# Optimization experiments

Measured on AMD Instinct MI355X. Metric: run time of the kernel, lower is better.

Reference implementation:

```python
import jax, jax.numpy as jnp
import numpy as np
import math

B, S, H = 2, 2048, 1024
NH, HD = 16, 64  # num heads, head dim; NH*HD == H


def setup_inputs() -> dict:
    key = jax.random.key(0)
    k1, k2, k3 = jax.random.split(key, 3)
    hidden_states = jax.random.normal(k1, (B, S, H), dtype=jnp.float32)
    # causal multiplicative mask [1,1,S,S], 1.0 where attending is allowed
    mask = jnp.tril(jnp.ones((S, S), dtype=jnp.float32))[None, None]
    W_qkv = jax.random.normal(k2, (H, 3 * H), dtype=jnp.float32) * (1.0 / math.sqrt(H))
    b_qkv = jnp.zeros((3 * H,), dtype=jnp.float32)
    W_out = jax.random.normal(k3, (H, H), dtype=jnp.float32) * (1.0 / math.sqrt(H))
    b_out = jnp.zeros((H,), dtype=jnp.float32)
    return {"hidden_states": hidden_states, "mask": mask, "W_qkv": W_qkv,
            "b_qkv": b_qkv, "W_out": W_out, "b_out": b_out}


def reference(hidden_states, mask, W_qkv, b_qkv, W_out, b_out):
    b, s, h = hidden_states.shape
    # fused QKV projection then split into contiguous thirds (split_tensor_along_last_dim)
    qkv = jnp.einsum('bsh,hd->bsd', hidden_states, W_qkv) + b_qkv
    q, k, v = jnp.split(qkv, 3, axis=-1)
    # [b, s, nh*hd] -> [b, nh, s, hd]
    def to_heads(t):
        return t.reshape(b, s, NH, HD).transpose(0, 2, 1, 3)
    q, k, v = to_heads(q), to_heads(k), to_heads(v)
    q = q / jnp.sqrt(jnp.float32(HD))  # scaling_attention_score=True
    scores = jnp.einsum('bhqd,bhkd->bhqk', q, k)  # [b,nh,s,s]
    # multiplicative mask + large-negative bias trick from standard_attention
    scores = scores * mask - 10000.0 * (1.0 - mask)
    probs = jax.nn.softmax(scores, axis=-1)
    ctx = jnp.einsum('bhqk,bhkd->bhqd', probs, v)
    ctx = ctx.transpose(0, 2, 1, 3).reshape(b, s, h)  # [b, s, nh*hd]
    return jnp.einsum('bsh,hd->bsd', ctx, W_out) + b_out
```

## Files before the change

### kernel.cpp

```cpp
#include <hip/hip_runtime.h>
#include <cstdint>
#include <cstddef>

#define NHEAD 16
#define HDIM 64
#define SEQ 2048
#define BATCH 2
#define HID 1024

typedef __bf16 bf16x8 __attribute__((ext_vector_type(8)));
typedef __bf16 bf16x2_t __attribute__((ext_vector_type(2)));
typedef float f32x4 __attribute__((ext_vector_type(4)));

__device__ __forceinline__ unsigned short f2bf(float f) {
    union { float f; unsigned u; } v; v.f = f;
    unsigned r = v.u + 0x7fffu + ((v.u >> 16) & 1u);
    return (unsigned short)(r >> 16);
}

__device__ __forceinline__ unsigned pk_bf16(float a, float b) {
#if __has_builtin(__builtin_amdgcn_cvt_pk_bf16_f32)
    bf16x2_t p = __builtin_amdgcn_cvt_pk_bf16_f32(a, b);
    return __builtin_bit_cast(unsigned, p);
#else
    return (unsigned)f2bf(a) | ((unsigned)f2bf(b) << 16);
#endif
}

__global__ __launch_bounds__(256) void convert_f32_bf16(
    const float* __restrict__ in, unsigned short* __restrict__ out, int n) {
    int i = (blockIdx.x * 256 + threadIdx.x) * 8;
    if (i >= n) return;
    float4 a = *(const float4*)(in + i);
    float4 b = *(const float4*)(in + i + 4);
    uint4 o;
    o.x = pk_bf16(a.x, a.y);
    o.y = pk_bf16(a.z, a.w);
    o.z = pk_bf16(b.x, b.y);
    o.w = pk_bf16(b.z, b.w);
    *(uint4*)(out + i) = o;
}

__global__ __launch_bounds__(256) void transpose_f32_bf16(
    const float* __restrict__ in, unsigned short* __restrict__ out, int R, int C) {
    __shared__ unsigned short T[64][72];
    int t = threadIdx.x;
    int c0 = blockIdx.x * 64, r0 = blockIdx.y * 64;
    for (int p = 0; p < 4; ++p) {
        int idx = (p * 256 + t) * 4;
        int row = idx >> 6, col = idx & 63;
        float4 v = *(const float4*)(in + (size_t)(r0 + row) * C + c0 + col);
        T[row][col + 0] = f2bf(v.x);
        T[row][col + 1] = f2bf(v.y);
        T[row][col + 2] = f2bf(v.z);
        T[row][col + 3] = f2bf(v.w);
    }
    __syncthreads();
    for (int p = 0; p < 4; ++p) {
        int idx = (p * 256 + t) * 4;
        int orow = idx >> 6, ocol = idx & 63;
        ushort4 u;
        u.x = T[ocol + 0][orow];
        u.y = T[ocol + 1][orow];
        u.z = T[ocol + 2][orow];
        u.w = T[ocol + 3][orow];
        *(ushort4*)(out + (size_t)(c0 + orow) * R + r0 + ocol) = u;
    }
}

#define GEMM_BODY(Aptr, Btptr, KDIM)                                                     \
    __shared__ unsigned short As[128][32];                                               \
    __shared__ unsigned short Bs[128][32];                                               \
    int t = threadIdx.x;                                                                 \
    int wave = t >> 6, lane = t & 63, ln = lane & 15, quad = lane >> 4;                  \
    int wm = wave >> 1, wn = wave & 1;                                                   \
    int m0 = blockIdx.y * 128, n0 = blockIdx.x * 128;                                    \
    int srow = lane >> 2, scol = (lane & 3) * 8;                                         \
    f32x4 zero4 = {0.f, 0.f, 0.f, 0.f};                                                  \
    f32x4 acc[4][4];                                                                     \
    for (int mi = 0; mi < 4; ++mi)                                                       \
        for (int ni = 0; ni < 4; ++ni) acc[mi][ni] = zero4;                              \
    for (int kt = 0; kt < (KDIM); kt += 32) {                                            \
        for (int p = 0; p < 2; ++p) {                                                    \
            int r0 = (wave * 2 + p) * 16 + srow;                                         \
            __builtin_amdgcn_global_load_lds(                                            \
                (const __attribute__((address_space(1))) void*)                          \
                    ((Aptr) + (size_t)(m0 + r0) * (KDIM) + kt + scol),                   \
                (__attribute__((address_space(3))) void*)&As[(wave * 2 + p) * 16][0],    \
                16, 0, 0);                                                               \
            __builtin_amdgcn_global_load_lds(                                            \
                (const __attribute__((address_space(1))) void*)                          \
                    ((Btptr) + (size_t)(n0 + r0) * (KDIM) + kt + scol),                  \
                (__attribute__((address_space(3))) void*)&Bs[(wave * 2 + p) * 16][0],    \
                16, 0, 0);                                                               \
        }                                                                                \
        __syncthreads();                                                                 \
        bf16x8 af[4], bfr[4];                                                            \
        for (int mi = 0; mi < 4; ++mi)                                                   \
            af[mi] = *(const bf16x8*)&As[wm * 64 + mi * 16 + ln][quad * 8];              \
        for (int ni = 0; ni < 4; ++ni)                                                   \
            bfr[ni] = *(const bf16x8*)&Bs[wn * 64 + ni * 16 + ln][quad * 8];             \
        for (int mi = 0; mi < 4; ++mi)                                                   \
            for (int ni = 0; ni < 4; ++ni)                                               \
                acc[mi][ni] = __builtin_amdgcn_mfma_f32_16x16x32_bf16(                   \
                    af[mi], bfr[ni], acc[mi][ni], 0, 0, 0);                              \
        __syncthreads();                                                                 \
    }

__global__ __launch_bounds__(256) void gemm_qkv(
    const unsigned short* __restrict__ A, const unsigned short* __restrict__ Bt,
    const float* __restrict__ bias,
    unsigned short* __restrict__ Qb, unsigned short* __restrict__ Kb,
    unsigned short* __restrict__ Vt) {
    GEMM_BODY(A, Bt, 1024)
    int nbase = n0 + wn * 64;
    for (int ni = 0; ni < 4; ++ni) {
        int gn = nbase + ni * 16 + ln;
        float bv = bias[gn];
        int third = gn >> 10;
        int rem = gn & 1023;
        int h = rem >> 6, d = rem & 63;
        if (third == 2) {
            for (int mi = 0; mi < 4; ++mi) {
                int gm0 = m0 + wm * 64 + mi * 16 + quad * 4;
                int b = gm0 >> 11, s = gm0 & 2047;
                size_t bh = (size_t)(b * NHEAD + h);
                uint2 u;
                u.x = pk_bf16(acc[mi][ni][0] + bv, acc[mi][ni][1] + bv);
                u.y = pk_bf16(acc[mi][ni][2] + bv, acc[mi][ni][3] + bv);
                *(uint2*)&Vt[(bh * HDIM + d) * SEQ + s] = u;
            }
        } else {
            unsigned short* dst = third == 0 ? Qb : Kb;
            float scale = third == 0 ? 0.1803368801111f : 1.0f;
            for (int mi = 0; mi < 4; ++mi) {
                for (int r = 0; r < 4; ++r) {
                    int gm = m0 + wm * 64 + mi * 16 + quad * 4 + r;
                    int b = gm >> 11, s = gm & 2047;
                    size_t bh = (size_t)(b * NHEAD + h);
                    dst[(bh * SEQ + s) * HDIM + d] = f2bf((acc[mi][ni][r] + bv) * scale);
                }
            }
        }
    }
}

__global__ __launch_bounds__(256) void gemm_out(
    const unsigned short* __restrict__ A, const unsigned short* __restrict__ Bt,
    const float* __restrict__ bias, float* __restrict__ C) {
    __shared__ unsigned short As[64][32];
    __shared__ unsigned short Bs[128][32];
    int t = threadIdx.x;
    int wave = t >> 6, lane = t & 63, ln = lane & 15, quad = lane >> 4;
    int wm = wave >> 1, wn = wave & 1;
    int m0 = blockIdx.y * 64, n0 = blockIdx.x * 128;
    int srow = lane >> 2, scol = (lane & 3) * 8;
    f32x4 zero4 = {0.f, 0.f, 0.f, 0.f};
    f32x4 acc[2][4];
    for (int mi = 0; mi < 2; ++mi)
        for (int ni = 0; ni < 4; ++ni) acc[mi][ni] = zero4;
    for (int kt = 0; kt < 1024; kt += 32) {
        for (int c = wave * 3; c < wave * 3 + 3; ++c) {
            if (c < 4) {
                __builtin_amdgcn_global_load_lds(
                    (const __attribute__((address_space(1))) void*)
                        (A + (size_t)(m0 + c * 16 + srow) * 1024 + kt + scol),
                    (__attribute__((address_space(3))) void*)&As[c * 16][0], 16, 0, 0);
            } else {
                int cb = c - 4;
                __builtin_amdgcn_global_load_lds(
                    (const __attribute__((address_space(1))) void*)
                        (Bt + (size_t)(n0 + cb * 16 + srow) * 1024 + kt + scol),
                    (__attribute__((address_space(3))) void*)&Bs[cb * 16][0], 16, 0, 0);
            }
        }
        __syncthreads();
        bf16x8 af[2], bfr[4];
        for (int mi = 0; mi < 2; ++mi)
            af[mi] = *(const bf16x8*)&As[wm * 32 + mi * 16 + ln][quad * 8];
        for (int ni = 0; ni < 4; ++ni)
            bfr[ni] = *(const bf16x8*)&Bs[wn * 64 + ni * 16 + ln][quad * 8];
        for (int mi = 0; mi < 2; ++mi)
            for (int ni = 0; ni < 4; ++ni)
                acc[mi][ni] = __builtin_amdgcn_mfma_f32_16x16x32_bf16(
                    af[mi], bfr[ni], acc[mi][ni], 0, 0, 0);
        __syncthreads();
    }
    for (int ni = 0; ni < 4; ++ni) {
        int gn = n0 + wn * 64 + ni * 16 + ln;
        float bv = bias[gn];
        for (int mi = 0; mi < 2; ++mi) {
            for (int r = 0; r < 4; ++r) {
                int gm = m0 + wm * 32 + mi * 16 + quad * 4 + r;
                C[(size_t)gm * HID + gn] = acc[mi][ni][r] + bv;
            }
        }
    }
}

__global__ __launch_bounds__(256) void flash_attn(
    const unsigned short* __restrict__ Qb, const unsigned short* __restrict__ Kb,
    const unsigned short* __restrict__ Vt, unsigned short* __restrict__ Ctx) {
    __shared__ unsigned short KsB[2][64][64];
    __shared__ unsigned short VsB[2][64][64];
    __shared__ unsigned short Ps[4][16][72];
    int tid = threadIdx.x;
    int wave = tid >> 6, lane = tid & 63, ln = lane & 15, quad = lane >> 4;
    int bh = blockIdx.y;
    int qiA = (bh < 16) ? blockIdx.x : (15 - blockIdx.x);
    int qiB = 31 - qiA;
    int q0A = qiA * 64, q0B = qiB * 64;
    const size_t baseQK = (size_t)bh * SEQ * HDIM;
    const size_t baseV = (size_t)bh * HDIM * SEQ;
    int b = bh >> 4, h = bh & 15;

    int rIn = lane >> 3;
    int gsw = ((lane & 7) ^ rIn) * 8;

    bf16x8 aqA0, aqA1, aqB0, aqB1;
    {
        const unsigned short* qp =
            Qb + baseQK + (size_t)(q0A + wave * 16 + ln) * HDIM + quad * 8;
        aqA0 = *(const bf16x8*)qp;
        aqA1 = *(const bf16x8*)(qp + 32);
        qp = Qb + baseQK + (size_t)(q0B + wave * 16 + ln) * HDIM + quad * 8;
        aqB0 = *(const bf16x8*)qp;
        aqB1 = *(const bf16x8*)(qp + 32);
    }

    auto prefetch = [&](int kj, int bi) {
        const unsigned short* kb = Kb + baseQK + (size_t)kj * 64 * HDIM;
        const unsigned short* vb = Vt + baseV + kj * 64;
        for (int c = wave; c < 8; c += 4) {
            __builtin_amdgcn_global_load_lds(
                (const __attribute__((address_space(1))) void*)(kb + (c * 8 + rIn) * HDIM + gsw),
                (__attribute__((address_space(3))) void*)&KsB[bi][c * 8][0], 16, 0, 0);
            __builtin_amdgcn_global_load_lds(
                (const __attribute__((address_space(1))) void*)(vb + (size_t)(c * 8 + rIn) * SEQ + gsw),
                (__attribute__((address_space(3))) void*)&VsB[bi][c * 8][0], 16, 0, 0);
        }
    };

    f32x4 zero4 = {0.f, 0.f, 0.f, 0.f};
    f32x4 oA[4], oB[4];
    float laccA = 0.f, laccB = 0.f;
    for (int i = 0; i < 4; ++i) { oA[i] = zero4; oB[i] = zero4; }

    auto epilogue = [&](f32x4* o, float lacc, int q0) {
        float sum = lacc;
        sum += __shfl_xor(sum, 16);
        sum += __shfl_xor(sum, 32);
        float linv = __builtin_amdgcn_rcpf(sum);
        size_t rowb = ((size_t)(b * SEQ + q0 + wave * 16 + ln)) * HID + h * 64;
        for (int ni = 0; ni < 4; ++ni) {
            uint2 u;
            u.x = pk_bf16(o[ni][0] * linv, o[ni][1] * linv);
            u.y = pk_bf16(o[ni][2] * linv, o[ni][3] * linv);
            *(uint2*)&Ctx[rowb + ni * 16 + quad * 4] = u;
        }
    };

    prefetch(0, 0);
    for (int k = 0; k <= qiB; ++k) {
        __syncthreads();
        if (k < qiB) prefetch(k + 1, (k + 1) & 1);
        int buf = k & 1;

        {
            f32x4 s4[4];
            for (int ni = 0; ni < 4; ++ni) s4[ni] = zero4;
            for (int kk = 0; kk < 2; ++kk) {
                bf16x8 bq = kk ? aqB1 : aqB0;
                for (int ni = 0; ni < 4; ++ni) {
                    bf16x8 ak = *(const bf16x8*)
                        &KsB[buf][ni * 16 + ln][((kk * 4 + quad) ^ (ln & 7)) * 8];
                    s4[ni] = __builtin_amdgcn_mfma_f32_16x16x32_bf16(ak, bq, s4[ni], 0, 0, 0);
                }
            }
            if (k == qiB) {
                for (int ni = 0; ni < 4; ++ni)
                    for (int r = 0; r < 4; ++r)
                        if (ni * 16 + quad * 4 + r > wave * 16 + ln) s4[ni][r] = -1.0e38f;
            }
            for (int ni = 0; ni < 4; ++ni) {
                float e0 = __builtin_amdgcn_exp2f(s4[ni][0]);
                float e1 = __builtin_amdgcn_exp2f(s4[ni][1]);
                float e2 = __builtin_amdgcn_exp2f(s4[ni][2]);
                float e3 = __builtin_amdgcn_exp2f(s4[ni][3]);
                laccB += (e0 + e1) + (e2 + e3);
                uint2 pk;
                pk.x = pk_bf16(e0, e1);
                pk.y = pk_bf16(e2, e3);
                *(uint2*)&Ps[wave][ln][ni * 16 + quad * 4] = pk;
            }
            for (int kk = 0; kk < 2; ++kk) {
                bf16x8 bp = *(const bf16x8*)&Ps[wave][ln][kk * 32 + quad * 8];
                for (int ni = 0; ni < 4; ++ni) {
                    bf16x8 av = *(const bf16x8*)
                        &VsB[buf][ni * 16 + ln][((kk * 4 + quad) ^ (ln & 7)) * 8];
                    oB[ni] = __builtin_amdgcn_mfma_f32_16x16x32_bf16(av, bp, oB[ni], 0, 0, 0);
                }
            }
        }

        if (k <= qiA) {
            f32x4 s4[4];
            for (int ni = 0; ni < 4; ++ni) s4[ni] = zero4;
            for (int kk = 0; kk < 2; ++kk) {
                bf16x8 bq = kk ? aqA1 : aqA0;
                for (int ni = 0; ni < 4; ++ni) {
                    bf16x8 ak = *(const bf16x8*)
                        &KsB[buf][ni * 16 + ln][((kk * 4 + quad) ^ (ln & 7)) * 8];
                    s4[ni] = __builtin_amdgcn_mfma_f32_16x16x32_bf16(ak, bq, s4[ni], 0, 0, 0);
                }
            }
            if (k == qiA) {
                for (int ni = 0; ni < 4; ++ni)
                    for (int r = 0; r < 4; ++r)
                        if (ni * 16 + quad * 4 + r > wave * 16 + ln) s4[ni][r] = -1.0e38f;
            }
            for (int ni = 0; ni < 4; ++ni) {
                float e0 = __builtin_amdgcn_exp2f(s4[ni][0]);
                float e1 = __builtin_amdgcn_exp2f(s4[ni][1]);
                float e2 = __builtin_amdgcn_exp2f(s4[ni][2]);
                float e3 = __builtin_amdgcn_exp2f(s4[ni][3]);
                laccA += (e0 + e1) + (e2 + e3);
                uint2 pk;
                pk.x = pk_bf16(e0, e1);
                pk.y = pk_bf16(e2, e3);
                *(uint2*)&Ps[wave][ln][ni * 16 + quad * 4] = pk;
            }
            for (int kk = 0; kk < 2; ++kk) {
                bf16x8 bp = *(const bf16x8*)&Ps[wave][ln][kk * 32 + quad * 8];
                for (int ni = 0; ni < 4; ++ni) {
                    bf16x8 av = *(const bf16x8*)
                        &VsB[buf][ni * 16 + ln][((kk * 4 + quad) ^ (ln & 7)) * 8];
                    oA[ni] = __builtin_amdgcn_mfma_f32_16x16x32_bf16(av, bp, oA[ni], 0, 0, 0);
                }
            }
            if (k == qiA) epilogue(oA, laccA, q0A);
        }
    }
    epilogue(oB, laccB, q0B);
}

extern "C" void kernel_launch(void* const* d_in, const int* in_sizes, int n_in,
                              void* d_out, int out_size, void* d_ws, size_t ws_size,
                              hipStream_t stream) {
    const float* X = (const float*)d_in[0];
    const float* Wqkv = (const float*)d_in[2];
    const float* bqkv = (const float*)d_in[3];
    const float* Wout = (const float*)d_in[4];
    const float* bout = (const float*)d_in[5];
    float* out = (float*)d_out;

    char* ws = (char*)d_ws;
    unsigned short* Xb  = (unsigned short*)(ws + 0);
    unsigned short* W1t = (unsigned short*)(ws + 8388608);
    unsigned short* W2t = (unsigned short*)(ws + 14680064);
    unsigned short* Qb  = (unsigned short*)(ws + 16777216);
    unsigned short* Kb  = (unsigned short*)(ws + 25165824);
    unsigned short* Vt  = (unsigned short*)(ws + 33554432);
    unsigned short* Ctx = (unsigned short*)(ws + 41943040);

    convert_f32_bf16<<<2048, 256, 0, stream>>>(X, Xb, 4194304);
    transpose_f32_bf16<<<dim3(48, 16), 256, 0, stream>>>(Wqkv, W1t, 1024, 3072);
    transpose_f32_bf16<<<dim3(16, 16), 256, 0, stream>>>(Wout, W2t, 1024, 1024);
    gemm_qkv<<<dim3(24, 32), 256, 0, stream>>>(Xb, W1t, bqkv, Qb, Kb, Vt);
    flash_attn<<<dim3(16, 32), 256, 0, stream>>>(Qb, Kb, Vt, Ctx);
    gemm_out<<<dim3(8, 64), 256, 0, stream>>>(Ctx, W2t, bout, out);
}
```

Baseline: 212.9 us.

## Double-buffer GEMM LDS tiles, merge prep kernels, split V transpose out

```diff
diff --git a/kernel.cpp b/kernel.cpp
--- a/kernel.cpp
+++ b/kernel.cpp
@@ -27,25 +27,11 @@
 #endif
 }
 
-__global__ __launch_bounds__(256) void convert_f32_bf16(
-    const float* __restrict__ in, unsigned short* __restrict__ out, int n) {
-    int i = (blockIdx.x * 256 + threadIdx.x) * 8;
-    if (i >= n) return;
-    float4 a = *(const float4*)(in + i);
-    float4 b = *(const float4*)(in + i + 4);
-    uint4 o;
-    o.x = pk_bf16(a.x, a.y);
-    o.y = pk_bf16(a.z, a.w);
-    o.z = pk_bf16(b.x, b.y);
-    o.w = pk_bf16(b.z, b.w);
-    *(uint4*)(out + i) = o;
-}
-
-__global__ __launch_bounds__(256) void transpose_f32_bf16(
-    const float* __restrict__ in, unsigned short* __restrict__ out, int R, int C) {
+__device__ __forceinline__ void transpose_tile(
+    const float* __restrict__ in, unsigned short* __restrict__ out,
+    int R, int C, int bx, int by, int t) {
     __shared__ unsigned short T[64][72];
-    int t = threadIdx.x;
-    int c0 = blockIdx.x * 64, r0 = blockIdx.y * 64;
+    int c0 = bx * 64, r0 = by * 64;
     for (int p = 0; p < 4; ++p) {
         int idx = (p * 256 + t) * 4;
         int row = idx >> 6, col = idx & 63;
@@ -68,9 +54,58 @@
     }
 }
 
-#define GEMM_BODY(Aptr, Btptr, KDIM)                                                     \
-    __shared__ unsigned short As[128][32];                                               \
-    __shared__ unsigned short Bs[128][32];                                               \
+__global__ __launch_bounds__(256) void prep(
+    const float* __restrict__ X, unsigned short* __restrict__ Xb,
+    const float* __restrict__ W1, unsigned short* __restrict__ W1t,
+    const float* __restrict__ W2, unsigned short* __restrict__ W2t) {
+    int blk = blockIdx.x, t = threadIdx.x;
+    if (blk < 2048) {
+        int i = (blk * 256 + t) * 8;
+        float4 a = *(const float4*)(X + i);
+        float4 b = *(const float4*)(X + i + 4);
+        uint4 o;
+        o.x = pk_bf16(a.x, a.y);
+        o.y = pk_bf16(a.z, a.w);
+        o.z = pk_bf16(b.x, b.y);
+        o.w = pk_bf16(b.z, b.w);
+        *(uint4*)(Xb + i) = o;
+    } else if (blk < 2816) {
+        int r = blk - 2048;
+        transpose_tile(W1, W1t, 1024, 3072, r % 48, r / 48, t);
+    } else {
+        int r = blk - 2816;
+        transpose_tile(W2, W2t, 1024, 1024, r % 16, r / 16, t);
+    }
+}
+
+__global__ __launch_bounds__(256) void transpose_v(
+    const unsigned short* __restrict__ in, unsigned short* __restrict__ out) {
+    __shared__ unsigned short T[64][72];
+    int t = threadIdx.x;
+    int s0 = blockIdx.x * 64, bh = blockIdx.y;
+    const unsigned short* ip = in + (size_t)bh * SEQ * HDIM;
+    unsigned short* op = out + (size_t)bh * HDIM * SEQ;
+    for (int p = 0; p < 2; ++p) {
+        int idx = (p * 256 + t) * 8;
+        int row = idx >> 6, col = idx & 63;
+        *(uint4*)&T[row][col] = *(const uint4*)(ip + (size_t)(s0 + row) * HDIM + col);
+    }
+    __syncthreads();
+    for (int p = 0; p < 4; ++p) {
+        int idx = (p * 256 + t) * 4;
+        int d = idx >> 6, c = idx & 63;
+        ushort4 u;
+        u.x = T[c + 0][d];
+        u.y = T[c + 1][d];
+        u.z = T[c + 2][d];
+        u.w = T[c + 3][d];
+        *(ushort4*)(op + (size_t)d * SEQ + s0 + c) = u;
+    }
+}
+
+#define GEMM_DB_BODY(Aptr, Btptr, KDIM)                                                  \
+    __shared__ unsigned short As[2][128][32];                                            \
+    __shared__ unsigned short Bs[2][128][32];                                            \
     int t = threadIdx.x;                                                                 \
     int wave = t >> 6, lane = t & 63, ln = lane & 15, quad = lane >> 4;                  \
     int wm = wave >> 1, wn = wave & 1;                                                   \
@@ -80,39 +115,44 @@
     f32x4 acc[4][4];                                                                     \
     for (int mi = 0; mi < 4; ++mi)                                                       \
         for (int ni = 0; ni < 4; ++ni) acc[mi][ni] = zero4;                              \
-    for (int kt = 0; kt < (KDIM); kt += 32) {                                            \
+    auto stage = [&](int kt, int bi) {                                                   \
         for (int p = 0; p < 2; ++p) {                                                    \
             int r0 = (wave * 2 + p) * 16 + srow;                                         \
             __builtin_amdgcn_global_load_lds(                                            \
                 (const __attribute__((address_space(1))) void*)                          \
                     ((Aptr) + (size_t)(m0 + r0) * (KDIM) + kt + scol),                   \
-                (__attribute__((address_space(3))) void*)&As[(wave * 2 + p) * 16][0],    \
+                (__attribute__((address_space(3))) void*)&As[bi][(wave * 2 + p) * 16][0],\
                 16, 0, 0);                                                               \
             __builtin_amdgcn_global_load_lds(                                            \
                 (const __attribute__((address_space(1))) void*)                          \
                     ((Btptr) + (size_t)(n0 + r0) * (KDIM) + kt + scol),                  \
-                (__attribute__((address_space(3))) void*)&Bs[(wave * 2 + p) * 16][0],    \
+                (__attribute__((address_space(3))) void*)&Bs[bi][(wave * 2 + p) * 16][0],\
                 16, 0, 0);                                                               \
         }                                                                                \
+    };                                                                                   \
+    stage(0, 0);                                                                         \
+    const int NIT = (KDIM) / 32;                                                         \
+    for (int it = 0; it < NIT; ++it) {                                                   \
         __syncthreads();                                                                 \
+        if (it + 1 < NIT) stage((it + 1) * 32, (it + 1) & 1);                            \
+        int bi = it & 1;                                                                 \
         bf16x8 af[4], bfr[4];                                                            \
         for (int mi = 0; mi < 4; ++mi)                                                   \
-            af[mi] = *(const bf16x8*)&As[wm * 64 + mi * 16 + ln][quad * 8];              \
+            af[mi] = *(const bf16x8*)&As[bi][wm * 64 + mi * 16 + ln][quad * 8];          \
         for (int ni = 0; ni < 4; ++ni)                                                   \
-            bfr[ni] = *(const bf16x8*)&Bs[wn * 64 + ni * 16 + ln][quad * 8];             \
+            bfr[ni] = *(const bf16x8*)&Bs[bi][wn * 64 + ni * 16 + ln][quad * 8];         \
         for (int mi = 0; mi < 4; ++mi)                                                   \
             for (int ni = 0; ni < 4; ++ni)                                               \
                 acc[mi][ni] = __builtin_amdgcn_mfma_f32_16x16x32_bf16(                   \
                     af[mi], bfr[ni], acc[mi][ni], 0, 0, 0);                              \
-        __syncthreads();                                                                 \
     }
 
 __global__ __launch_bounds__(256) void gemm_qkv(
     const unsigned short* __restrict__ A, const unsigned short* __restrict__ Bt,
     const float* __restrict__ bias,
     unsigned short* __restrict__ Qb, unsigned short* __restrict__ Kb,
-    unsigned short* __restrict__ Vt) {
-    GEMM_BODY(A, Bt, 1024)
+    unsigned short* __restrict__ Vtmp) {
+    GEMM_DB_BODY(A, Bt, 1024)
     int nbase = n0 + wn * 64;
     for (int ni = 0; ni < 4; ++ni) {
         int gn = nbase + ni * 16 + ln;
@@ -120,26 +160,14 @@
         int third = gn >> 10;
         int rem = gn & 1023;
         int h = rem >> 6, d = rem & 63;
-        if (third == 2) {
-            for (int mi = 0; mi < 4; ++mi) {
-                int gm0 = m0 + wm * 64 + mi * 16 + quad * 4;
-                int b = gm0 >> 11, s = gm0 & 2047;
+        unsigned short* dst = third == 0 ? Qb : (third == 1 ? Kb : Vtmp);
+        float scale = third == 0 ? 0.1803368801111f : 1.0f;
+        for (int mi = 0; mi < 4; ++mi) {
+            for (int r = 0; r < 4; ++r) {
+                int gm = m0 + wm * 64 + mi * 16 + quad * 4 + r;
+                int b = gm >> 11, s = gm & 2047;
                 size_t bh = (size_t)(b * NHEAD + h);
-                uint2 u;
-                u.x = pk_bf16(acc[mi][ni][0] + bv, acc[mi][ni][1] + bv);
-                u.y = pk_bf16(acc[mi][ni][2] + bv, acc[mi][ni][3] + bv);
-                *(uint2*)&Vt[(bh * HDIM + d) * SEQ + s] = u;
-            }
-        } else {
-            unsigned short* dst = third == 0 ? Qb : Kb;
-            float scale = third == 0 ? 0.1803368801111f : 1.0f;
-            for (int mi = 0; mi < 4; ++mi) {
-                for (int r = 0; r < 4; ++r) {
-                    int gm = m0 + wm * 64 + mi * 16 + quad * 4 + r;
-                    int b = gm >> 11, s = gm & 2047;
-                    size_t bh = (size_t)(b * NHEAD + h);
-                    dst[(bh * SEQ + s) * HDIM + d] = f2bf((acc[mi][ni][r] + bv) * scale);
-                }
+                dst[(bh * SEQ + s) * HDIM + d] = f2bf((acc[mi][ni][r] + bv) * scale);
             }
         }
     }
@@ -148,8 +176,8 @@
 __global__ __launch_bounds__(256) void gemm_out(
     const unsigned short* __restrict__ A, const unsigned short* __restrict__ Bt,
     const float* __restrict__ bias, float* __restrict__ C) {
-    __shared__ unsigned short As[64][32];
-    __shared__ unsigned short Bs[128][32];
+    __shared__ unsigned short As[2][64][32];
+    __shared__ unsigned short Bs[2][128][32];
     int t = threadIdx.x;
     int wave = t >> 6, lane = t & 63, ln = lane & 15, quad = lane >> 4;
     int wm = wave >> 1, wn = wave & 1;
@@ -159,32 +187,36 @@
     f32x4 acc[2][4];
     for (int mi = 0; mi < 2; ++mi)
         for (int ni = 0; ni < 4; ++ni) acc[mi][ni] = zero4;
-    for (int kt = 0; kt < 1024; kt += 32) {
+    auto stage = [&](int kt, int bi) {
         for (int c = wave * 3; c < wave * 3 + 3; ++c) {
             if (c < 4) {
                 __builtin_amdgcn_global_load_lds(
                     (const __attribute__((address_space(1))) void*)
                         (A + (size_t)(m0 + c * 16 + srow) * 1024 + kt + scol),
-                    (__attribute__((address_space(3))) void*)&As[c * 16][0], 16, 0, 0);
+                    (__attribute__((address_space(3))) void*)&As[bi][c * 16][0], 16, 0, 0);
             } else {
                 int cb = c - 4;
                 __builtin_amdgcn_global_load_lds(
                     (const __attribute__((address_space(1))) void*)
                         (Bt + (size_t)(n0 + cb * 16 + srow) * 1024 + kt + scol),
-                    (__attribute__((address_space(3))) void*)&Bs[cb * 16][0], 16, 0, 0);
-            }
-        }
+                    (__attribute__((address_space(3))) void*)&Bs[bi][cb * 16][0], 16, 0, 0);
+            }
+        }
+    };
+    stage(0, 0);
+    for (int it = 0; it < 32; ++it) {
         __syncthreads();
+        if (it + 1 < 32) stage((it + 1) * 32, (it + 1) & 1);
+        int bi = it & 1;
         bf16x8 af[2], bfr[4];
         for (int mi = 0; mi < 2; ++mi)
-            af[mi] = *(const bf16x8*)&As[wm * 32 + mi * 16 + ln][quad * 8];
+            af[mi] = *(const bf16x8*)&As[bi][wm * 32 + mi * 16 + ln][quad * 8];
         for (int ni = 0; ni < 4; ++ni)
-            bfr[ni] = *(const bf16x8*)&Bs[wn * 64 + ni * 16 + ln][quad * 8];
+            bfr[ni] = *(const bf16x8*)&Bs[bi][wn * 64 + ni * 16 + ln][quad * 8];
         for (int mi = 0; mi < 2; ++mi)
             for (int ni = 0; ni < 4; ++ni)
                 acc[mi][ni] = __builtin_amdgcn_mfma_f32_16x16x32_bf16(
                     af[mi], bfr[ni], acc[mi][ni], 0, 0, 0);
-        __syncthreads();
     }
     for (int ni = 0; ni < 4; ++ni) {
         int gn = n0 + wn * 64 + ni * 16 + ln;
@@ -355,18 +387,18 @@
     float* out = (float*)d_out;
 
     char* ws = (char*)d_ws;
-    unsigned short* Xb  = (unsigned short*)(ws + 0);
-    unsigned short* W1t = (unsigned short*)(ws + 8388608);
-    unsigned short* W2t = (unsigned short*)(ws + 14680064);
-    unsigned short* Qb  = (unsigned short*)(ws + 16777216);
-    unsigned short* Kb  = (unsigned short*)(ws + 25165824);
-    unsigned short* Vt  = (unsigned short*)(ws + 33554432);
-    unsigned short* Ctx = (unsigned short*)(ws + 41943040);
-
-    convert_f32_bf16<<<2048, 256, 0, stream>>>(X, Xb, 4194304);
-    transpose_f32_bf16<<<dim3(48, 16), 256, 0, stream>>>(Wqkv, W1t, 1024, 3072);
-    transpose_f32_bf16<<<dim3(16, 16), 256, 0, stream>>>(Wout, W2t, 1024, 1024);
-    gemm_qkv<<<dim3(24, 32), 256, 0, stream>>>(Xb, W1t, bqkv, Qb, Kb, Vt);
+    unsigned short* Xb   = (unsigned short*)(ws + 0);
+    unsigned short* Vt   = (unsigned short*)(ws + 0);
+    unsigned short* W1t  = (unsigned short*)(ws + 8388608);
+    unsigned short* W2t  = (unsigned short*)(ws + 14680064);
+    unsigned short* Qb   = (unsigned short*)(ws + 16777216);
+    unsigned short* Kb   = (unsigned short*)(ws + 25165824);
+    unsigned short* Vtmp = (unsigned short*)(ws + 33554432);
+    unsigned short* Ctx  = (unsigned short*)(ws + 41943040);
+
+    prep<<<3072, 256, 0, stream>>>(X, Xb, Wqkv, W1t, Wout, W2t);
+    gemm_qkv<<<dim3(24, 32), 256, 0, stream>>>(Xb, W1t, bqkv, Qb, Kb, Vtmp);
+    transpose_v<<<dim3(32, 32), 256, 0, stream>>>(Vtmp, Vt);
     flash_attn<<<dim3(16, 32), 256, 0, stream>>>(Qb, Kb, Vt, Ctx);
     gemm_out<<<dim3(8, 64), 256, 0, stream>>>(Ctx, W2t, bout, out);
 }
```

After: 208.9 us. No clear change (-1.9%).
